# Performance work log

Hardware: AMD Instinct MI355X
Metric: run time of the kernel (lower is better)

## Reference

```python
import jax, jax.numpy as jnp
import numpy as np

EMBED_DIM = 2048
NUM_Q_HEADS = 32
NUM_KV_HEADS = 8
HEAD_DIM = EMBED_DIM // NUM_Q_HEADS
N_REP = NUM_Q_HEADS // NUM_KV_HEADS
B, T = 2, 2048


def setup_inputs() -> dict:
    key = jax.random.key(0)
    ks = jax.random.split(key, 10)
    C = EMBED_DIM
    kv_dim = NUM_KV_HEADS * HEAD_DIM
    s = 1.0 / np.sqrt(C)
    return {
        "x": jax.random.normal(ks[0], (B, T, C), dtype=jnp.float32),
        "mask": jnp.tril(jnp.ones((1, 1, T, T), dtype=bool)),
        "Wq": jax.random.normal(ks[1], (C, C), dtype=jnp.float32) * s,
        "bq": jnp.zeros((C,), dtype=jnp.float32),
        "Wk": jax.random.normal(ks[2], (C, kv_dim), dtype=jnp.float32) * s,
        "bk": jnp.zeros((kv_dim,), dtype=jnp.float32),
        "Wv": jax.random.normal(ks[3], (C, kv_dim), dtype=jnp.float32) * s,
        "bv": jnp.zeros((kv_dim,), dtype=jnp.float32),
        "Wo": jax.random.normal(ks[4], (C, C), dtype=jnp.float32) * s,
        "bo": jnp.zeros((C,), dtype=jnp.float32),
    }


def reference(x, mask, Wq, bq, Wk, bk, Wv, bv, Wo, bo):
    b, t, c = x.shape
    # projections
    q = (x @ Wq + bq).reshape(b, t, NUM_Q_HEADS, HEAD_DIM).transpose(0, 2, 1, 3)   # [B,Hq,T,D]
    k = (x @ Wk + bk).reshape(b, t, NUM_KV_HEADS, HEAD_DIM).transpose(0, 2, 1, 3)  # [B,Hkv,T,D]
    v = (x @ Wv + bv).reshape(b, t, NUM_KV_HEADS, HEAD_DIM).transpose(0, 2, 1, 3)
    # repeat KV heads to match query heads (same math as expand+reshape)
    k = jnp.repeat(k, N_REP, axis=1)  # [B,Hq,T,D]
    v = jnp.repeat(v, N_REP, axis=1)
    scores = jnp.einsum("bhqd,bhkd->bhqk", q, k) / np.sqrt(HEAD_DIM)
    scores = jnp.where(mask, scores, -jnp.inf)
    attn = jax.nn.softmax(scores, axis=-1)
    out = jnp.einsum("bhqk,bhkd->bhqd", attn, v)  # [B,Hq,T,D]
    out = out.transpose(0, 2, 1, 3).reshape(b, t, c)
    return out @ Wo + bo
```

## Files before the change

### kernel.cpp

```cpp
#include <hip/hip_runtime.h>
#include <stdint.h>

typedef __attribute__((ext_vector_type(8))) short bf16x8;
typedef __attribute__((ext_vector_type(4))) float f32x4;

#define LOG2E 1.44269504088896f
#define T_SEQ 2048

__device__ __forceinline__ float bf2f(short s) {
    unsigned u = ((unsigned)(unsigned short)s) << 16;
    float f; __builtin_memcpy(&f, &u, 4); return f;
}
__device__ __forceinline__ short f2bf(float f) {
    unsigned u; __builtin_memcpy(&u, &f, 4);
    u = (u + 0x7FFFu + ((u >> 16) & 1u)) >> 16;
    return (short)u;
}
__device__ __forceinline__ short f2bf_trunc(float f) {
    unsigned u; __builtin_memcpy(&u, &f, 4);
    return (short)(u >> 16);
}

#define GLDS(g, l) __builtin_amdgcn_global_load_lds( \
    (const __attribute__((address_space(1))) void*)(g), \
    (__attribute__((address_space(3))) void*)(l), 16, 0, 0)

__device__ __forceinline__ void fence_barrier() {
    asm volatile("" ::: "memory");
    __builtin_amdgcn_s_barrier();
    asm volatile("" ::: "memory");
}

__global__ void detect_k(const unsigned short* __restrict__ x, int* __restrict__ flag) {
    int lane = threadIdx.x;
    int cnt = 0;
    for (int i = lane; i < 2048; i += 64) {
        int e = (x[i] >> 7) & 0xFF;
        if (e >= 0xC0) cnt++;
    }
    cnt += __shfl_xor(cnt, 1);
    cnt += __shfl_xor(cnt, 2);
    cnt += __shfl_xor(cnt, 4);
    cnt += __shfl_xor(cnt, 8);
    cnt += __shfl_xor(cnt, 16);
    cnt += __shfl_xor(cnt, 32);
    if (lane == 0) { flag[0] = (cnt >= 32) ? 1 : 0; flag[1] = 0; }
}

__global__ __launch_bounds__(256) void convert_k(
    const void* __restrict__ in, short* __restrict__ out, int n,
    const int* __restrict__ flag)
{
    int i = (blockIdx.x * 256 + threadIdx.x) * 8;
    if (i >= n) return;
    bf16x8 v;
    if (*flag) {
        const float* f = (const float*)in + i;
        #pragma unroll
        for (int j = 0; j < 8; ++j) v[j] = f2bf(f[j]);
    } else {
        v = *(const bf16x8*)((const short*)in + i);
    }
    *(bf16x8*)(out + i) = v;
}

__global__ __launch_bounds__(256) void convert4_k(
    const void* __restrict__ b0, const void* __restrict__ b1,
    const void* __restrict__ b2, const void* __restrict__ b3,
    short* __restrict__ o0, short* __restrict__ o1,
    short* __restrict__ o2, short* __restrict__ o3,
    const int* __restrict__ flag)
{
    int i = (blockIdx.x * 256 + threadIdx.x) * 8;
    const void* in; short* out; int off;
    if      (i < 2048) { in = b0; out = o0; off = i; }
    else if (i < 2560) { in = b1; out = o1; off = i - 2048; }
    else if (i < 3072) { in = b2; out = o2; off = i - 2560; }
    else if (i < 5120) { in = b3; out = o3; off = i - 3072; }
    else return;
    bf16x8 v;
    if (*flag) {
        const float* f = (const float*)in + off;
        #pragma unroll
        for (int j = 0; j < 8; ++j) v[j] = f2bf(f[j]);
    } else {
        v = *(const bf16x8*)((const short*)in + off);
    }
    *(bf16x8*)(out + off) = v;
}

__global__ __launch_bounds__(256) void transpose_k(
    const void* __restrict__ in_, short* __restrict__ out,
    int R, int ldi, long ibstride, long obstride, const int* __restrict__ flag)
{
    short* ob = out + (long)blockIdx.z * obstride;
    int c = blockIdx.x * 256 + threadIdx.x;
    int r0 = blockIdx.y * 64;
    int fp32 = *flag;
    if (fp32) {
        const float* ib = (const float*)in_ + (long)blockIdx.z * ibstride;
        for (int rr = 0; rr < 64; rr += 8) {
            bf16x8 v;
            #pragma unroll
            for (int j = 0; j < 8; ++j) v[j] = f2bf(ib[(long)(r0 + rr + j) * ldi + c]);
            *(bf16x8*)(ob + (long)c * R + r0 + rr) = v;
        }
    } else {
        const short* ib = (const short*)in_ + (long)blockIdx.z * ibstride;
        for (int rr = 0; rr < 64; rr += 8) {
            bf16x8 v;
            #pragma unroll
            for (int j = 0; j < 8; ++j) v[j] = ib[(long)(r0 + rr + j) * ldi + c];
            *(bf16x8*)(ob + (long)c * R + r0 + rr) = v;
        }
    }
}

template <int BN>
__global__ __launch_bounds__(512, 1) void gemm256_k(
    const short* __restrict__ A, const short* __restrict__ Bt,
    const short* __restrict__ bias1, int nsplit,
    short* __restrict__ C, short* __restrict__ C2, int n2,
    float* __restrict__ Cf, const int* __restrict__ flag,
    int M, int N, int K)
{
    constexpr int NT = BN / 64;
    __shared__ short a_lds[2][256 * 32];
    __shared__ short b_lds[2][BN * 32];
    const int tid = threadIdx.x;
    const int wave = tid >> 6, lane = tid & 63;
    const int quad = lane >> 4, l16 = lane & 15;
    const int m0 = blockIdx.y * 256, n0 = blockIdx.x * BN;
    const int wm = (wave >> 2) * 128;
    const int wn = (wave & 3) * (BN / 4);

    const int rA0 = tid >> 2,         kA0 = (tid & 3) ^ ((rA0 >> 1) & 3);
    const int rA1 = (512 + tid) >> 2, kA1 = (tid & 3) ^ ((rA1 >> 1) & 3);
    const long aoff0 = (long)(m0 + rA0) * K + kA0 * 8;
    const long aoff1 = (long)(m0 + rA1) * K + kA1 * 8;
    const long boff0 = (long)(n0 + rA0) * K + kA0 * 8;
    const long boff1 = (long)(n0 + rA1) * K + kA1 * 8;

    int aro[8], bro[NT];
    #pragma unroll
    for (int mt = 0; mt < 8; ++mt) {
        int ra = wm + mt * 16 + l16;
        aro[mt] = ra * 32 + (quad ^ ((ra >> 1) & 3)) * 8;
    }
    #pragma unroll
    for (int nt = 0; nt < NT; ++nt) {
        int rb = wn + nt * 16 + l16;
        bro[nt] = rb * 32 + (quad ^ ((rb >> 1) & 3)) * 8;
    }

    f32x4 acc[8][NT];
    #pragma unroll
    for (int i = 0; i < 8; ++i)
        #pragma unroll
        for (int j = 0; j < NT; ++j)
            acc[i][j] = (f32x4){0.f, 0.f, 0.f, 0.f};

    const int nk = K >> 5;
    GLDS(A + aoff0, &a_lds[0][0] + wave * 512);
    GLDS(A + aoff1, &a_lds[0][0] + 4096 + wave * 512);
    GLDS(Bt + boff0, &b_lds[0][0] + wave * 512);
    if constexpr (BN == 256) GLDS(Bt + boff1, &b_lds[0][0] + 4096 + wave * 512);

    for (int t = 0; t < nk; ++t) {
        const int p = t & 1;
        const long kn = (long)((t + 1 < nk) ? t + 1 : t) * 32;
        short* an = &a_lds[p ^ 1][0];
        short* bn = &b_lds[p ^ 1][0];
        GLDS(A + aoff0 + kn, an + wave * 512);
        GLDS(A + aoff1 + kn, an + 4096 + wave * 512);
        GLDS(Bt + boff0 + kn, bn + wave * 512);
        if constexpr (BN == 256) GLDS(Bt + boff1 + kn, bn + 4096 + wave * 512);

        if constexpr (BN == 256) asm volatile("s_waitcnt vmcnt(4)" ::: "memory");
        else                     asm volatile("s_waitcnt vmcnt(3)" ::: "memory");
        fence_barrier();

        const short* ac = &a_lds[p][0];
        const short* bc = &b_lds[p][0];
        bf16x8 bfr[NT], af[4];
        #pragma unroll
        for (int nt = 0; nt < NT; ++nt) bfr[nt] = *(const bf16x8*)(bc + bro[nt]);
        #pragma unroll
        for (int mt = 0; mt < 4; ++mt) af[mt] = *(const bf16x8*)(ac + aro[mt]);
        __builtin_amdgcn_s_setprio(1);
        #pragma unroll
        for (int mt = 0; mt < 4; ++mt)
            #pragma unroll
            for (int nt = 0; nt < NT; ++nt)
                acc[mt][nt] = __builtin_amdgcn_mfma_f32_16x16x32_bf16(
                    af[mt], bfr[nt], acc[mt][nt], 0, 0, 0);
        __builtin_amdgcn_s_setprio(0);
        #pragma unroll
        for (int mt = 0; mt < 4; ++mt) af[mt] = *(const bf16x8*)(ac + aro[mt + 4]);
        __builtin_amdgcn_s_setprio(1);
        #pragma unroll
        for (int mt = 0; mt < 4; ++mt)
            #pragma unroll
            for (int nt = 0; nt < NT; ++nt)
                acc[mt + 4][nt] = __builtin_amdgcn_mfma_f32_16x16x32_bf16(
                    af[mt], bfr[nt], acc[mt + 4][nt], 0, 0, 0);
        __builtin_amdgcn_s_setprio(0);
        asm volatile("s_waitcnt lgkmcnt(0)" ::: "memory");
        fence_barrier();
    }

    const int f32o = Cf ? *flag : 0;
    #pragma unroll
    for (int nt = 0; nt < NT; ++nt) {
        int col = n0 + wn + nt * 16 + l16;
        float bb = bf2f(bias1[col < nsplit ? col : 0]);
        #pragma unroll
        for (int mt = 0; mt < 8; ++mt)
            #pragma unroll
            for (int r = 0; r < 4; ++r) {
                int row = m0 + wm + mt * 16 + quad * 4 + r;
                float val = acc[mt][nt][r] + bb;
                if (f32o) {
                    Cf[(long)row * N + col] = val;
                } else if (C2) {
                    if (col < n2) C[(long)row * n2 + col] = f2bf(val);
                    else          C2[(long)row * (N - n2) + (col - n2)] = f2bf(val);
                } else {
                    C[(long)row * N + col] = f2bf(val);
                }
            }
    }
}

#define PLD 68
__global__ __launch_bounds__(256, 4) void attn_k(
    const short* __restrict__ Qf, const short* __restrict__ KVf,
    const short* __restrict__ Vt, short* __restrict__ Attn)
{
    __shared__ short k_lds[64 * PLD];
    __shared__ short vt_lds[64 * PLD];
    __shared__ short p_lds[4 * 32 * PLD];
    const int tid = threadIdx.x;
    const int wave = tid >> 6, lane = tid & 63;
    const int quad = lane >> 4, l16 = lane & 15;

    const int id = blockIdx.x;
    const int bh = id & 63;
    const int w = id >> 6;
    const int QTMAP[16] = {15,13,11,9, 0,2,4,6, 14,12,10,8, 1,3,5,7};
    const int qt = QTMAP[w];
    const int b = bh >> 5, h = bh & 31, hkv = h >> 2;
    const int q0 = qt * 128;
    const int nsteps = 2 * (qt + 1);

    bf16x8 aq[2][2];
    #pragma unroll
    for (int mt = 0; mt < 2; ++mt) {
        const short* qp = Qf + ((long)(b * T_SEQ + q0 + wave * 32 + mt * 16 + l16) * 2048
                                + h * 64 + quad * 8);
        aq[mt][0] = *(const bf16x8*)qp;
        aq[mt][1] = *(const bf16x8*)(qp + 32);
        #pragma unroll
        for (int j = 0; j < 8; ++j) {
            aq[mt][0][j] = f2bf(bf2f(aq[mt][0][j]) * 0.125f);
            aq[mt][1][j] = f2bf(bf2f(aq[mt][1][j]) * 0.125f);
        }
    }

    bf16x8 onesf;
    {
        short o = (l16 == 0) ? (short)0x3F80 : (short)0;
        #pragma unroll
        for (int j = 0; j < 8; ++j) onesf[j] = o;
    }

    f32x4 o_acc[2][4];
    f32x4 l_acc[2];
    #pragma unroll
    for (int mt = 0; mt < 2; ++mt) {
        l_acc[mt] = (f32x4){0.f, 0.f, 0.f, 0.f};
        #pragma unroll
        for (int dt = 0; dt < 4; ++dt) o_acc[mt][dt] = (f32x4){0.f, 0.f, 0.f, 0.f};
    }

    const int cA = tid, cB = 256 + tid;
    const int tA = cA >> 3, chA = cA & 7;
    const int tB = cB >> 3, chB = cB & 7;
    const short* kgA = KVf + ((long)(b * T_SEQ + tA) * 1024 + hkv * 64 + chA * 8);
    const short* kgB = KVf + ((long)(b * T_SEQ + tB) * 1024 + hkv * 64 + chB * 8);
    const short* vgA = Vt + ((long)((b * 8 + hkv) * 64 + tA) * 2048 + chA * 8);
    const short* vgB = Vt + ((long)((b * 8 + hkv) * 64 + tB) * 2048 + chB * 8);

    const int rowq0 = q0 + wave * 32 + quad * 4;
    short* pw = p_lds + (wave * 32 + quad * 4) * PLD + l16;
    const short* pr = p_lds + (wave * 32 + l16) * PLD + quad * 8;

    bf16x8 kA = *(const bf16x8*)(kgA);
    bf16x8 kB = *(const bf16x8*)(kgB);
    bf16x8 vA = *(const bf16x8*)(vgA);
    bf16x8 vB = *(const bf16x8*)(vgB);

    for (int s = 0; s < nsteps; ++s) {
        const int kt0 = s * 64;
        const int ktn = ((s + 1 < nsteps) ? (s + 1) : s) * 64;
        __syncthreads();
        *(bf16x8*)(k_lds + tA * PLD + chA * 8) = kA;
        *(bf16x8*)(k_lds + tB * PLD + chB * 8) = kB;
        *(bf16x8*)(vt_lds + tA * PLD + chA * 8) = vA;
        *(bf16x8*)(vt_lds + tB * PLD + chB * 8) = vB;
        kA = *(const bf16x8*)(kgA + (long)ktn * 1024);
        kB = *(const bf16x8*)(kgB + (long)ktn * 1024);
        vA = *(const bf16x8*)(vgA + ktn);
        vB = *(const bf16x8*)(vgB + ktn);
        __syncthreads();

        const int masked = (kt0 >= q0);
        #pragma unroll
        for (int nt = 0; nt < 4; ++nt) {
            bf16x8 bk0 = *(const bf16x8*)(k_lds + (nt * 16 + l16) * PLD + quad * 8);
            bf16x8 bk1 = *(const bf16x8*)(k_lds + (nt * 16 + l16) * PLD + 32 + quad * 8);
            #pragma unroll
            for (int mt = 0; mt < 2; ++mt) {
                f32x4 z = (f32x4){0.f, 0.f, 0.f, 0.f};
                z = __builtin_amdgcn_mfma_f32_16x16x32_bf16(aq[mt][0], bk0, z, 0, 0, 0);
                z = __builtin_amdgcn_mfma_f32_16x16x32_bf16(aq[mt][1], bk1, z, 0, 0, 0);
                if (!masked) {
                    #pragma unroll
                    for (int r = 0; r < 4; ++r)
                        z[r] = exp2f(fmaf(z[r], LOG2E, -16.0f));
                } else {
                    const int rowq = rowq0 + mt * 16;
                    const int tcol = kt0 + nt * 16 + l16;
                    #pragma unroll
                    for (int r = 0; r < 4; ++r) {
                        float e = exp2f(fmaf(z[r], LOG2E, -16.0f));
                        z[r] = (tcol <= rowq + r) ? e : 0.0f;
                    }
                }
                #pragma unroll
                for (int r = 0; r < 4; ++r)
                    pw[mt * 16 * PLD + r * PLD + nt * 16] = f2bf_trunc(z[r]);
            }
        }

        bf16x8 ap[2][2];
        #pragma unroll
        for (int mt = 0; mt < 2; ++mt) {
            ap[mt][0] = *(const bf16x8*)(pr + mt * 16 * PLD);
            ap[mt][1] = *(const bf16x8*)(pr + mt * 16 * PLD + 32);
        }
        #pragma unroll
        for (int dt = 0; dt < 4; ++dt) {
            bf16x8 bv0 = *(const bf16x8*)(vt_lds + (dt * 16 + l16) * PLD + quad * 8);
            bf16x8 bv1 = *(const bf16x8*)(vt_lds + (dt * 16 + l16) * PLD + 32 + quad * 8);
            #pragma unroll
            for (int mt = 0; mt < 2; ++mt) {
                o_acc[mt][dt] = __builtin_amdgcn_mfma_f32_16x16x32_bf16(ap[mt][0], bv0, o_acc[mt][dt], 0, 0, 0);
                o_acc[mt][dt] = __builtin_amdgcn_mfma_f32_16x16x32_bf16(ap[mt][1], bv1, o_acc[mt][dt], 0, 0, 0);
            }
        }
        #pragma unroll
        for (int mt = 0; mt < 2; ++mt) {
            l_acc[mt] = __builtin_amdgcn_mfma_f32_16x16x32_bf16(ap[mt][0], onesf, l_acc[mt], 0, 0, 0);
            l_acc[mt] = __builtin_amdgcn_mfma_f32_16x16x32_bf16(ap[mt][1], onesf, l_acc[mt], 0, 0, 0);
        }
    }

    #pragma unroll
    for (int mt = 0; mt < 2; ++mt)
        #pragma unroll
        for (int r = 0; r < 4; ++r) {
            const float linv = 1.0f / __shfl(l_acc[mt][r], quad << 4);
            const int rowo = q0 + wave * 32 + mt * 16 + quad * 4 + r;
            short* ap = Attn + (long)(b * T_SEQ + rowo) * 2048 + h * 64 + l16;
            #pragma unroll
            for (int dt = 0; dt < 4; ++dt)
                ap[dt * 16] = f2bf(o_acc[mt][dt][r] * linv);
        }
}

extern "C" void kernel_launch(void* const* d_in, const int* in_sizes, int n_in,
                              void* d_out, int out_size, void* d_ws, size_t ws_size,
                              hipStream_t stream) {
    const void* x  = d_in[0];
    const void* Wq = d_in[2];
    const void* bq = d_in[3];
    const void* Wk = d_in[4];
    const void* bk = d_in[5];
    const void* Wv = d_in[6];
    const void* bv = d_in[7];
    const void* Wo = d_in[8];
    const void* bo = d_in[9];

    short* ws    = (short*)d_ws;
    int*   flags = (int*)ws;
    short* base  = ws + 16;
    short* xb    = base;
    short* Wq_t  = xb + (long)8388608;
    short* Wkv_t = Wq_t + (long)4194304;
    short* regB  = base + (long)17039360;
    short* bqb   = regB;
    short* bkb   = bqb + 2048;
    short* bvb   = bkb + 512;
    short* bob   = bvb + 512;
    short* Wo_t  = bob + 2048;
    short* Qf    = Wo_t + (long)4194304;
    short* KVf   = Qf + (long)8388608;
    short* Vtp   = KVf + (long)4194304;
    short* Attn  = Vtp + (long)2097152;

    detect_k<<<1, 64, 0, stream>>>((const unsigned short*)x, flags);

    convert_k<<<4096, 256, 0, stream>>>(x, xb, 4096 * 2048, flags);
    convert4_k<<<3, 256, 0, stream>>>(bq, bk, bv, bo, bqb, bkb, bvb, bob, flags);

    transpose_k<<<dim3(8, 32, 1), 256, 0, stream>>>(Wq, Wq_t, 2048, 2048, 0L, 0L, flags);
    transpose_k<<<dim3(2, 32, 1), 256, 0, stream>>>(Wk, Wkv_t, 2048, 512, 0L, 0L, flags);
    transpose_k<<<dim3(2, 32, 1), 256, 0, stream>>>(Wv, Wkv_t + (long)512 * 2048, 2048, 512, 0L, 0L, flags);
    transpose_k<<<dim3(8, 32, 1), 256, 0, stream>>>(Wo, Wo_t, 2048, 2048, 0L, 0L, flags);

    gemm256_k<256><<<dim3(12, 16), 512, 0, stream>>>(xb, Wq_t, bqb, 3072,
                                                     Qf, KVf, 2048, nullptr, flags,
                                                     4096, 3072, 2048);

    transpose_k<<<dim3(2, 32, 2), 256, 0, stream>>>(KVf + 512, Vtp, 2048, 1024,
                                                    (long)2048 * 1024, (long)512 * 2048, flags + 1);

    attn_k<<<1024, 256, 0, stream>>>(Qf, KVf, Vtp, Attn);

    gemm256_k<128><<<dim3(16, 16), 512, 0, stream>>>(Attn, Wo_t, bob, 2048,
                                                     (short*)d_out, nullptr, 0,
                                                     (float*)d_out, flags,
                                                     4096, 2048, 2048);
}
```

Before: 469.2 us.

## Use single-buffered 128x128 tile GEMM for fused QKV projection

Adds a new gemm_bt kernel with 128x128 tiles, 256 threads, a single LDS buffer and two barriers per K step, and uses it for the QKV projection in place of the double-buffered 256x256 gemm256_k. The grid grows from 192 to 768 blocks, which fills more of the GPU's compute units and avoids a partial wave. In exchange the kernel loses the global-load/MFMA overlap that double buffering gave and gets less operand reuse per tile.

```diff
diff --git a/kernel.cpp b/kernel.cpp
--- a/kernel.cpp
+++ b/kernel.cpp
@@ -113,6 +113,94 @@
             for (int j = 0; j < 8; ++j) v[j] = ib[(long)(r0 + rr + j) * ldi + c];
             *(bf16x8*)(ob + (long)c * R + r0 + rr) = v;
         }
+    }
+}
+
+#define BK 32
+__global__ __launch_bounds__(256) void gemm_bt(
+    const short* __restrict__ A, const short* __restrict__ Bt,
+    const short* __restrict__ bias1, int nsplit,
+    short* __restrict__ C, short* __restrict__ C2, int n2,
+    float* __restrict__ Cf, const int* __restrict__ flag,
+    int M, int N, int K)
+{
+    __shared__ short a_lds[128 * BK];
+    __shared__ short b_lds[128 * BK];
+    const int tid = threadIdx.x;
+    const int wave = tid >> 6, lane = tid & 63;
+    const int quad = lane >> 4, l16 = lane & 15;
+    const int m0 = blockIdx.y * 128, n0 = blockIdx.x * 128;
+    const int wm = (wave >> 1) * 64, wn = (wave & 1) * 64;
+
+    const int c0 = wave * 64 + lane;
+    const int c1 = 256 + c0;
+    const int row0 = c0 >> 2, kc0 = (c0 & 3) ^ ((row0 >> 1) & 3);
+    const int row1 = c1 >> 2, kc1 = (c1 & 3) ^ ((row1 >> 1) & 3);
+    const long aoff0 = (long)(m0 + row0) * K + kc0 * 8;
+    const long aoff1 = (long)(m0 + row1) * K + kc1 * 8;
+    const long boff0 = (long)(n0 + row0) * K + kc0 * 8;
+    const long boff1 = (long)(n0 + row1) * K + kc1 * 8;
+    short* alp0 = a_lds + (wave * 64) * 8;
+    short* alp1 = a_lds + (256 + wave * 64) * 8;
+    short* blp0 = b_lds + (wave * 64) * 8;
+    short* blp1 = b_lds + (256 + wave * 64) * 8;
+
+    int aro[4], bro[4];
+    #pragma unroll
+    for (int t = 0; t < 4; ++t) {
+        int ra = wm + t * 16 + l16;
+        aro[t] = ra * BK + (quad ^ ((ra >> 1) & 3)) * 8;
+        int rb = wn + t * 16 + l16;
+        bro[t] = rb * BK + (quad ^ ((rb >> 1) & 3)) * 8;
+    }
+
+    f32x4 acc[4][4];
+    #pragma unroll
+    for (int i = 0; i < 4; ++i)
+        #pragma unroll
+        for (int j = 0; j < 4; ++j)
+            acc[i][j] = (f32x4){0.f, 0.f, 0.f, 0.f};
+
+    for (int k0 = 0; k0 < K; k0 += BK) {
+        __syncthreads();
+        GLDS(A + aoff0 + k0, alp0);
+        GLDS(A + aoff1 + k0, alp1);
+        GLDS(Bt + boff0 + k0, blp0);
+        GLDS(Bt + boff1 + k0, blp1);
+        __syncthreads();
+        bf16x8 af[4], bfr[4];
+        #pragma unroll
+        for (int t = 0; t < 4; ++t) af[t] = *(const bf16x8*)(a_lds + aro[t]);
+        #pragma unroll
+        for (int t = 0; t < 4; ++t) bfr[t] = *(const bf16x8*)(b_lds + bro[t]);
+        #pragma unroll
+        for (int mt = 0; mt < 4; ++mt)
+            #pragma unroll
+            for (int nt = 0; nt < 4; ++nt)
+                acc[mt][nt] = __builtin_amdgcn_mfma_f32_16x16x32_bf16(
+                    af[mt], bfr[nt], acc[mt][nt], 0, 0, 0);
+    }
+
+    const int f32o = Cf ? *flag : 0;
+    #pragma unroll
+    for (int nt = 0; nt < 4; ++nt) {
+        int col = n0 + wn + nt * 16 + l16;
+        float bb = bf2f(bias1[col < nsplit ? col : 0]);
+        #pragma unroll
+        for (int mt = 0; mt < 4; ++mt)
+            #pragma unroll
+            for (int r = 0; r < 4; ++r) {
+                int row = m0 + wm + mt * 16 + quad * 4 + r;
+                float val = acc[mt][nt][r] + bb;
+                if (f32o) {
+                    Cf[(long)row * N + col] = val;
+                } else if (C2) {
+                    if (col < n2) C[(long)row * n2 + col] = f2bf(val);
+                    else          C2[(long)row * (N - n2) + (col - n2)] = f2bf(val);
+                } else {
+                    C[(long)row * N + col] = f2bf(val);
+                }
+            }
     }
 }
 
@@ -419,9 +507,9 @@
     transpose_k<<<dim3(2, 32, 1), 256, 0, stream>>>(Wv, Wkv_t + (long)512 * 2048, 2048, 512, 0L, 0L, flags);
     transpose_k<<<dim3(8, 32, 1), 256, 0, stream>>>(Wo, Wo_t, 2048, 2048, 0L, 0L, flags);
 
-    gemm256_k<256><<<dim3(12, 16), 512, 0, stream>>>(xb, Wq_t, bqb, 3072,
-                                                     Qf, KVf, 2048, nullptr, flags,
-                                                     4096, 3072, 2048);
+    gemm_bt<<<dim3(24, 32), 256, 0, stream>>>(xb, Wq_t, bqb, 3072,
+                                              Qf, KVf, 2048, nullptr, flags,
+                                              4096, 3072, 2048);
 
     transpose_k<<<dim3(2, 32, 2), 256, 0, stream>>>(KVf + 512, Vtp, 2048, 1024,
                                                     (long)2048 * 1024, (long)512 * 2048, flags + 1);
```

Result: no change. 460.4 us (-1.9%).
